# Performance work log

Hardware: AMD Instinct MI355X
Metric: run time of the kernel (lower is better)

The kernel has to match this reference:

```python
import jax, jax.numpy as jnp
import numpy as np

TWO_PI = 2.0 * np.pi
EPS = 1e-12  # torch F.normalize eps


def setup_inputs() -> dict:
    key = jax.random.key(0)
    ks = jax.random.split(key, 12)
    B, NS, G = 16, 128, 20000
    P, S, E, T = 200, 128, 128, 50
    return {
        "x_genes": jax.random.normal(ks[0], (B, NS, G), jnp.float32),
        "tissue_idx": jax.random.randint(ks[1], (B, NS), 0, T, jnp.int32),
        "pathway_idx": jax.random.randint(ks[2], (P, S), 0, G, jnp.int32),
        "W_proj": jax.random.normal(ks[3], (P, E, S), jnp.float32) * (1.0 / np.sqrt(S)),
        "b_proj": jax.random.normal(ks[4], (P, E), jnp.float32) * 0.02,
        "tissue_table": jax.random.normal(ks[5], (T, E), jnp.float32),
        "W1": jax.random.normal(ks[6], (E, 32), jnp.float32) * (1.0 / np.sqrt(E)),
        "b1": jax.random.normal(ks[7], (32,), jnp.float32) * 0.02,
        "W2": jax.random.normal(ks[8], (32, 2), jnp.float32) * (1.0 / np.sqrt(32)),
        "b2": jax.random.normal(ks[9], (2,), jnp.float32) * 0.02,
        "Wdec": jax.random.normal(ks[10], (2, G), jnp.float32) * (1.0 / np.sqrt(2.0)),
        "bdec": jax.random.normal(ks[11], (G,), jnp.float32) * 0.02,
    }


def _l2norm(v):
    n = jnp.sqrt(jnp.sum(v * v, axis=-1, keepdims=True))
    return v / jnp.maximum(n, EPS)


def reference(x_genes, tissue_idx, pathway_idx, W_proj, b_proj, tissue_table,
              W1, b1, W2, b2, Wdec, bdec):
    B, NS, G = x_genes.shape
    x = x_genes.reshape(-1, G)            # [N, G], N = B*NS
    t = tissue_idx.reshape(-1)            # [N]

    # Pathway tokenizer: gather gene subsets + per-pathway linear (grouped GEMM)
    xg = x[:, pathway_idx]                # [N, P, S]
    H = jax.nn.relu(jnp.einsum('nps,pes->npe', xg, W_proj) + b_proj)  # [N, P, E]

    # Single-query attention with tissue embedding as query
    Q = tissue_table[t]                   # [N, E]
    scale = 1.0 / np.sqrt(H.shape[-1])
    scores = jnp.einsum('ne,npe->np', Q, H) * scale   # [N, P]
    attn = jax.nn.softmax(scores, axis=-1)
    context = jnp.einsum('np,npe->ne', attn, H)       # [N, E]

    # to_latent MLP (dropout=0 / eval)
    h = jax.nn.relu(context @ W1 + b1)
    pc = h @ W2 + b2                      # [N, 2]
    pcn = _l2norm(pc)
    ang = jnp.remainder(jnp.arctan2(pcn[:, 1], pcn[:, 0]) + TWO_PI, TWO_PI)

    # decode + normalize
    rec = _l2norm(pcn @ Wdec + bdec)      # [N, G]

    return (pcn.reshape(B, NS, 2), ang.reshape(B, NS), rec.reshape(B, NS, G))
```

## Files before the change

kernel.cpp:

```cpp
#include <hip/hip_runtime.h>
#include <cmath>

#define GG 20000
#define NN 2048
#define PP 200
#define SS 128
#define EE 128
#define TN 128
#define NPAIR 100

typedef __bf16 bf16x8 __attribute__((ext_vector_type(8)));
typedef float f32x16 __attribute__((ext_vector_type(16)));
typedef unsigned short u16x8 __attribute__((ext_vector_type(8)));

__device__ __align__(16) unsigned g_xTi[(size_t)GG * NN];
__device__ __align__(16) unsigned short g_Wsw[(size_t)PP * 32768];
__device__ float g_ctxp[(size_t)NN * NPAIR * EE];
__device__ float g_mT[NPAIR * NN];
__device__ float g_lT[NPAIR * NN];

__device__ __forceinline__ unsigned short f2bf(float f) {
  unsigned u = __builtin_bit_cast(unsigned, f);
  return (unsigned short)((u + 0x7FFFu + ((u >> 16) & 1u)) >> 16);
}
__device__ __forceinline__ float bf2f(unsigned short h) {
  return __builtin_bit_cast(float, (unsigned)h << 16);
}
__device__ __forceinline__ unsigned packhl(float f) {
  unsigned short h = f2bf(f);
  unsigned short l = f2bf(f - bf2f(h));
  return (unsigned)h | ((unsigned)l << 16);
}

__global__ __launch_bounds__(256) void transpose_convert_kernel(
    const float* __restrict__ x)
{
  __shared__ float tile[64][65];
  const int g0 = blockIdx.x * 64;
  const int n0 = blockIdx.y * 64;
  const int t = threadIdx.x;
  {
    const int gq = t & 15, nl4 = t >> 4;
    #pragma unroll
    for (int k = 0; k < 4; ++k) {
      int nl = nl4 + 16 * k;
      int g = g0 + gq * 4;
      if (g + 3 < GG) {
        float4 v = *(const float4*)&x[(size_t)(n0 + nl) * GG + g];
        tile[gq * 4 + 0][nl] = v.x;
        tile[gq * 4 + 1][nl] = v.y;
        tile[gq * 4 + 2][nl] = v.z;
        tile[gq * 4 + 3][nl] = v.w;
      }
    }
  }
  __syncthreads();
  {
    const int nq = t & 15, gl4 = t >> 4;
    #pragma unroll
    for (int k = 0; k < 4; ++k) {
      int gl = gl4 + 16 * k;
      int g = g0 + gl;
      if (g < GG) {
        uint4 v;
        v.x = packhl(tile[gl][nq * 4 + 0]);
        v.y = packhl(tile[gl][nq * 4 + 1]);
        v.z = packhl(tile[gl][nq * 4 + 2]);
        v.w = packhl(tile[gl][nq * 4 + 3]);
        *(uint4*)&g_xTi[(size_t)g * NN + n0 + nq * 4] = v;
      }
    }
  }
}

__global__ __launch_bounds__(256) void wconvert_kernel(const float* __restrict__ Wp)
{
  unsigned v = blockIdx.x * 256 + threadIdx.x;
  const int si = v & 7;
  const int slp = (v >> 3) & 7;
  const int e = (v >> 6) & 127;
  const int ch = (v >> 13) & 1;
  const int p = v >> 14;
  const int slot = slp ^ (e & 7);
  const int s = ch * 64 + slot * 8 + si;
  float f = Wp[((size_t)p * EE + e) * SS + s];
  unsigned short h = f2bf(f);
  unsigned short l = f2bf(f - bf2f(h));
  size_t base = (size_t)(p * 2 + ch) * 16384 + e * 64 + slp * 8 + si;
  g_Wsw[base] = h;
  g_Wsw[base + 8192] = l;
}

__device__ __forceinline__ void load16(unsigned* xr, const int* sidx_lds,
                                       int sbase, int kh, int ncol) {
  #pragma unroll
  for (int ks2 = 0; ks2 < 2; ++ks2)
    #pragma unroll
    for (int j = 0; j < 8; ++j) {
      int s = (sbase + ks2) * 16 + kh * 8 + j;
      xr[ks2 * 8 + j] = g_xTi[(size_t)sidx_lds[s] * NN + ncol];
    }
}

__device__ __forceinline__ void compute2ks(const unsigned short* wb,
                                           const unsigned* xr, f32x16 (&acc)[4],
                                           int ksbase, int nl, int kh) {
  #pragma unroll
  for (int ks2 = 0; ks2 < 2; ++ks2) {
    const int ks = ksbase + ks2;
    const unsigned short* wAh = wb + (ks >> 2) * 16384;
    const unsigned short* wAl = wAh + 8192;
    u16x8 bhu, blu;
    #pragma unroll
    for (int j = 0; j < 8; ++j) {
      unsigned v = xr[ks2 * 8 + j];
      bhu[j] = (unsigned short)(v & 0xffffu);
      blu[j] = (unsigned short)(v >> 16);
    }
    bf16x8 bh = __builtin_bit_cast(bf16x8, bhu);
    bf16x8 bl = __builtin_bit_cast(bf16x8, blu);
    #pragma unroll
    for (int et = 0; et < 4; ++et) {
      const int e = et * 32 + nl;
      const int slp = ((ks & 3) * 2 + kh) ^ (e & 7);
      bf16x8 ah = __builtin_bit_cast(bf16x8, *(const uint4*)(wAh + e * 64 + slp * 8));
      bf16x8 al = __builtin_bit_cast(bf16x8, *(const uint4*)(wAl + e * 64 + slp * 8));
      acc[et] = __builtin_amdgcn_mfma_f32_32x32x16_bf16(ah, bh, acc[et], 0, 0, 0);
      acc[et] = __builtin_amdgcn_mfma_f32_32x32x16_bf16(ah, bl, acc[et], 0, 0, 0);
      acc[et] = __builtin_amdgcn_mfma_f32_32x32x16_bf16(al, bh, acc[et], 0, 0, 0);
    }
  }
}

__device__ __forceinline__ void pathway_body(
    int p, unsigned short* wbuf, int* sidx, float* sbp,
    const int* __restrict__ pidx, const float* __restrict__ bp,
    const float* __restrict__ tt, int tid_n,
    int t, int w, int ln, int nl, int kh, int ncol,
    f32x16 (&h)[4], float& s_out)
{
  __syncthreads();
  if (t < 128) sidx[t] = pidx[p * SS + t];
  else         sbp[t - 128] = bp[p * EE + (t - 128)];
  {
    const unsigned short* src = g_Wsw + (size_t)p * 32768 + w * 8192 + ln * 8;
    unsigned short* dst = wbuf + w * 8192;
    #pragma unroll
    for (int j = 0; j < 16; ++j) {
      __builtin_amdgcn_global_load_lds(
          (const __attribute__((address_space(1))) unsigned int*)(src + j * 512),
          (__attribute__((address_space(3))) unsigned int*)(dst + j * 512), 16, 0, 0);
    }
  }
  __syncthreads();

  #pragma unroll
  for (int et = 0; et < 4; ++et)
    #pragma unroll
    for (int r = 0; r < 16; ++r) h[et][r] = 0.f;

  unsigned xa[16], xb[16];
  load16(xa, sidx, 0, kh, ncol);
  load16(xb, sidx, 2, kh, ncol);
  compute2ks(wbuf, xa, h, 0, nl, kh);
  load16(xa, sidx, 4, kh, ncol);
  compute2ks(wbuf, xb, h, 2, nl, kh);
  load16(xb, sidx, 6, kh, ncol);
  compute2ks(wbuf, xa, h, 4, nl, kh);
  compute2ks(wbuf, xb, h, 6, nl, kh);

  const float4* qp = (const float4*)(tt + (size_t)tid_n * EE);
  float scr = 0.f;
  #pragma unroll
  for (int et = 0; et < 4; ++et)
    #pragma unroll
    for (int rq = 0; rq < 4; ++rq) {
      int e0 = et * 32 + rq * 8 + kh * 4;
      float4 q4 = qp[e0 >> 2];
      float4 b4 = *(const float4*)&sbp[e0];
      float h0 = fmaxf(h[et][rq * 4 + 0] + b4.x, 0.f);
      float h1 = fmaxf(h[et][rq * 4 + 1] + b4.y, 0.f);
      float h2 = fmaxf(h[et][rq * 4 + 2] + b4.z, 0.f);
      float h3 = fmaxf(h[et][rq * 4 + 3] + b4.w, 0.f);
      h[et][rq * 4 + 0] = h0; h[et][rq * 4 + 1] = h1;
      h[et][rq * 4 + 2] = h2; h[et][rq * 4 + 3] = h3;
      scr += h0 * q4.x + h1 * q4.y + h2 * q4.z + h3 * q4.w;
    }
  scr += __shfl_xor(scr, 32);
  s_out = scr * 0.08838834764831845f;
}

__global__ __launch_bounds__(256, 2) void proj_mfma_kernel(
    const int* __restrict__ tidx, const int* __restrict__ pidx,
    const float* __restrict__ bp, const float* __restrict__ tt)
{
  __shared__ __align__(16) unsigned short wbuf[32768];
  __shared__ int sidx[SS];
  __shared__ float sbp[EE];

  const int t = threadIdx.x;
  const int w = t >> 6;
  const int ln = t & 63;
  const int nl = ln & 31;
  const int kh = ln >> 5;
  const int n0 = blockIdx.x * TN;
  const int pair = blockIdx.y;
  const int ncol = n0 + w * 32 + nl;
  const int tid_n = tidx[ncol];

  f32x16 h0[4], h1[4];
  float s0, s1;
  pathway_body(pair * 2 + 0, wbuf, sidx, sbp, pidx, bp, tt, tid_n,
               t, w, ln, nl, kh, ncol, h0, s0);
  pathway_body(pair * 2 + 1, wbuf, sidx, sbp, pidx, bp, tt, tid_n,
               t, w, ln, nl, kh, ncol, h1, s1);

  const float m = fmaxf(s0, s1);
  const float w0 = expf(s0 - m);
  const float w1 = expf(s1 - m);
  const float lsum = w0 + w1;
  #pragma unroll
  for (int et = 0; et < 4; ++et)
    #pragma unroll
    for (int r = 0; r < 16; ++r)
      h0[et][r] = w0 * h0[et][r] + w1 * h1[et][r];

  __syncthreads();
  float* tb = ((float*)wbuf) + w * (32 * 128);
  #pragma unroll
  for (int et = 0; et < 4; ++et)
    #pragma unroll
    for (int rq = 0; rq < 4; ++rq) {
      int slot = et * 8 + rq * 2 + kh;
      float4 v = make_float4(h0[et][rq * 4 + 0], h0[et][rq * 4 + 1],
                             h0[et][rq * 4 + 2], h0[et][rq * 4 + 3]);
      *(float4*)&tb[nl * 128 + ((slot ^ nl) << 2)] = v;
    }
  __syncthreads();
  {
    const int rrow = ln >> 1, eh = (ln & 1) * 16;
    const int nn = n0 + w * 32 + rrow;
    float* dst = g_ctxp + ((size_t)nn * NPAIR + pair) * EE + eh * 4;
    const float* srcrow = tb + rrow * 128;
    #pragma unroll
    for (int k = 0; k < 16; ++k) {
      int slot = eh + k;
      *(float4*)&dst[k * 4] = *(const float4*)&srcrow[(slot ^ rrow) << 2];
    }
  }
  if (ln < 32) {
    g_mT[pair * NN + ncol] = m;
    g_lT[pair * NN + ncol] = lsum;
  }
}

__global__ __launch_bounds__(256) void combine_rec_kernel(
    const float* __restrict__ W1, const float* __restrict__ b1,
    const float* __restrict__ W2, const float* __restrict__ b2,
    const float* __restrict__ Wdec, const float* __restrict__ bdec,
    float* __restrict__ out)
{
  const int n = blockIdx.x;
  const int t = threadIdx.x;
  __shared__ float ws[NPAIR];
  __shared__ float ctx2[2][EE];
  __shared__ float r1[4], r2[4];
  __shared__ float hsh[32];
  __shared__ float qsh[2];
  __shared__ float red[4];

  float mv = (t < NPAIR) ? g_mT[t * NN + n] : -1e30f;
  float lv = (t < NPAIR) ? g_lT[t * NN + n] : 0.f;
  float M = mv;
  #pragma unroll
  for (int off = 32; off >= 1; off >>= 1) M = fmaxf(M, __shfl_xor(M, off));
  if ((t & 63) == 0) r1[t >> 6] = M;
  __syncthreads();
  M = fmaxf(fmaxf(r1[0], r1[1]), fmaxf(r1[2], r1[3]));
  float wv = (t < NPAIR) ? expf(mv - M) : 0.f;
  if (t < NPAIR) ws[t] = wv;
  float Lp = wv * lv;
  #pragma unroll
  for (int off = 32; off >= 1; off >>= 1) Lp += __shfl_xor(Lp, off);
  if ((t & 63) == 0) r2[t >> 6] = Lp;
  __syncthreads();
  const float L = r2[0] + r2[1] + r2[2] + r2[3];

  {
    const int e = t & 127, hf = t >> 7;
    const float* base = g_ctxp + ((size_t)n * NPAIR + hf * 50) * EE + e;
    float c = 0.f;
    #pragma unroll 5
    for (int s = 0; s < 50; ++s) c += ws[hf * 50 + s] * base[(size_t)s * EE];
    ctx2[hf][e] = c;
  }
  __syncthreads();
  const float invL = 1.f / L;
  if (t < 32) {
    float h = 0.f;
    for (int e = 0; e < EE; ++e) h += (ctx2[0][e] + ctx2[1][e]) * W1[e * 32 + t];
    hsh[t] = fmaxf(h * invL + b1[t], 0.f);
  }
  __syncthreads();
  if (t == 0) {
    float p0 = b2[0], p1 = b2[1];
    #pragma unroll
    for (int k = 0; k < 32; ++k) { p0 += hsh[k] * W2[k * 2]; p1 += hsh[k] * W2[k * 2 + 1]; }
    float inv = 1.f / fmaxf(sqrtf(p0 * p0 + p1 * p1), 1e-12f);
    float q0 = p0 * inv, q1 = p1 * inv;
    const float PI2 = 6.2831853071795864769f;
    float ang = atan2f(q1, q0) + PI2;
    if (ang >= PI2) ang -= PI2;
    out[n * 2 + 0] = q0;
    out[n * 2 + 1] = q1;
    out[2 * NN + n] = ang;
    qsh[0] = q0; qsh[1] = q1;
  }
  __syncthreads();
  const float q0 = qsh[0], q1 = qsh[1];

  float ss = 0.f;
  for (int i = t; i < GG / 4; i += 256) {
    float4 w0 = *(const float4*)&Wdec[i * 4];
    float4 w1 = *(const float4*)&Wdec[GG + i * 4];
    float4 bd = *(const float4*)&bdec[i * 4];
    float v0 = q0 * w0.x + q1 * w1.x + bd.x;
    float v1 = q0 * w0.y + q1 * w1.y + bd.y;
    float v2 = q0 * w0.z + q1 * w1.z + bd.z;
    float v3 = q0 * w0.w + q1 * w1.w + bd.w;
    ss += v0 * v0 + v1 * v1 + v2 * v2 + v3 * v3;
  }
  #pragma unroll
  for (int off = 32; off >= 1; off >>= 1) ss += __shfl_xor(ss, off);
  if ((t & 63) == 0) red[t >> 6] = ss;
  __syncthreads();
  const float inv = 1.f / fmaxf(sqrtf(red[0] + red[1] + red[2] + red[3]), 1e-12f);

  float* orec = out + 3 * NN + (size_t)n * GG;
  for (int i = t; i < GG / 4; i += 256) {
    float4 w0 = *(const float4*)&Wdec[i * 4];
    float4 w1 = *(const float4*)&Wdec[GG + i * 4];
    float4 bd = *(const float4*)&bdec[i * 4];
    float4 o;
    o.x = (q0 * w0.x + q1 * w1.x + bd.x) * inv;
    o.y = (q0 * w0.y + q1 * w1.y + bd.y) * inv;
    o.z = (q0 * w0.z + q1 * w1.z + bd.z) * inv;
    o.w = (q0 * w0.w + q1 * w1.w + bd.w) * inv;
    *(float4*)&orec[i * 4] = o;
  }
}

extern "C" void kernel_launch(void* const* d_in, const int* in_sizes, int n_in,
                              void* d_out, int out_size, void* d_ws, size_t ws_size,
                              hipStream_t stream) {
  (void)in_sizes; (void)n_in; (void)out_size; (void)d_ws; (void)ws_size;
  const float* x    = (const float*)d_in[0];
  const int*   tidx = (const int*)  d_in[1];
  const int*   pidx = (const int*)  d_in[2];
  const float* Wp   = (const float*)d_in[3];
  const float* bp   = (const float*)d_in[4];
  const float* tt   = (const float*)d_in[5];
  const float* W1   = (const float*)d_in[6];
  const float* b1   = (const float*)d_in[7];
  const float* W2   = (const float*)d_in[8];
  const float* b2   = (const float*)d_in[9];
  const float* Wdec = (const float*)d_in[10];
  const float* bdec = (const float*)d_in[11];
  float* out = (float*)d_out;

  dim3 gridT((GG + 63) / 64, NN / 64, 1);
  transpose_convert_kernel<<<gridT, 256, 0, stream>>>(x);
  wconvert_kernel<<<(PP * 16384) / 256, 256, 0, stream>>>(Wp);

  dim3 gridA(NN / TN, NPAIR, 1);
  proj_mfma_kernel<<<gridA, 256, 0, stream>>>(tidx, pidx, bp, tt);

  combine_rec_kernel<<<NN, 256, 0, stream>>>(W1, b1, W2, b2, Wdec, bdec, out);
}
```

Baseline: 320.6 us.

## Process eight pathways per block with online softmax to shrink partial context buffer

Each projection block now loops over eight pathways instead of two, keeping a running max, sum and weighted context in registers (online softmax). The partial-context buffer and max/sum arrays drop from 100 to 25 slices per sample, which cuts global write traffic in the projection kernel and read traffic in the combine kernel. The cost is a grid with a quarter as many blocks (16x25 = 400), so there is less parallelism for the MI355X's CUs and each block runs longer and more serially.

```diff
diff --git a/kernel.cpp b/kernel.cpp
--- a/kernel.cpp
+++ b/kernel.cpp
@@ -7,7 +7,8 @@
 #define SS 128
 #define EE 128
 #define TN 128
-#define NPAIR 100
+#define TPP 8
+#define NOCT 25
 
 typedef __bf16 bf16x8 __attribute__((ext_vector_type(8)));
 typedef float f32x16 __attribute__((ext_vector_type(16)));
@@ -15,9 +16,9 @@
 
 __device__ __align__(16) unsigned g_xTi[(size_t)GG * NN];
 __device__ __align__(16) unsigned short g_Wsw[(size_t)PP * 32768];
-__device__ float g_ctxp[(size_t)NN * NPAIR * EE];
-__device__ float g_mT[NPAIR * NN];
-__device__ float g_lT[NPAIR * NN];
+__device__ float g_ctxp[(size_t)NN * NOCT * EE];
+__device__ float g_mT[NOCT * NN];
+__device__ float g_lT[NOCT * NN];
 
 __device__ __forceinline__ unsigned short f2bf(float f) {
   unsigned u = __builtin_bit_cast(unsigned, f);
@@ -204,26 +205,33 @@
   const int nl = ln & 31;
   const int kh = ln >> 5;
   const int n0 = blockIdx.x * TN;
-  const int pair = blockIdx.y;
+  const int oct = blockIdx.y;
   const int ncol = n0 + w * 32 + nl;
   const int tid_n = tidx[ncol];
 
-  f32x16 h0[4], h1[4];
-  float s0, s1;
-  pathway_body(pair * 2 + 0, wbuf, sidx, sbp, pidx, bp, tt, tid_n,
-               t, w, ln, nl, kh, ncol, h0, s0);
-  pathway_body(pair * 2 + 1, wbuf, sidx, sbp, pidx, bp, tt, tid_n,
-               t, w, ln, nl, kh, ncol, h1, s1);
-
-  const float m = fmaxf(s0, s1);
-  const float w0 = expf(s0 - m);
-  const float w1 = expf(s1 - m);
-  const float lsum = w0 + w1;
+  f32x16 ctx[4];
   #pragma unroll
   for (int et = 0; et < 4; ++et)
     #pragma unroll
-    for (int r = 0; r < 16; ++r)
-      h0[et][r] = w0 * h0[et][r] + w1 * h1[et][r];
+    for (int r = 0; r < 16; ++r) ctx[et][r] = 0.f;
+  float m_r = -1e30f, l_r = 0.f;
+
+  f32x16 h[4];
+  float s;
+  for (int pp = 0; pp < TPP; ++pp) {
+    pathway_body(oct * TPP + pp, wbuf, sidx, sbp, pidx, bp, tt, tid_n,
+                 t, w, ln, nl, kh, ncol, h, s);
+    const float mn = fmaxf(m_r, s);
+    const float f = expf(m_r - mn);
+    const float wg = expf(s - mn);
+    l_r = l_r * f + wg;
+    m_r = mn;
+    #pragma unroll
+    for (int et = 0; et < 4; ++et)
+      #pragma unroll
+      for (int r = 0; r < 16; ++r)
+        ctx[et][r] = ctx[et][r] * f + wg * h[et][r];
+  }
 
   __syncthreads();
   float* tb = ((float*)wbuf) + w * (32 * 128);
@@ -232,15 +240,15 @@
     #pragma unroll
     for (int rq = 0; rq < 4; ++rq) {
       int slot = et * 8 + rq * 2 + kh;
-      float4 v = make_float4(h0[et][rq * 4 + 0], h0[et][rq * 4 + 1],
-                             h0[et][rq * 4 + 2], h0[et][rq * 4 + 3]);
+      float4 v = make_float4(ctx[et][rq * 4 + 0], ctx[et][rq * 4 + 1],
+                             ctx[et][rq * 4 + 2], ctx[et][rq * 4 + 3]);
       *(float4*)&tb[nl * 128 + ((slot ^ nl) << 2)] = v;
     }
   __syncthreads();
   {
     const int rrow = ln >> 1, eh = (ln & 1) * 16;
     const int nn = n0 + w * 32 + rrow;
-    float* dst = g_ctxp + ((size_t)nn * NPAIR + pair) * EE + eh * 4;
+    float* dst = g_ctxp + ((size_t)nn * NOCT + oct) * EE + eh * 4;
     const float* srcrow = tb + rrow * 128;
     #pragma unroll
     for (int k = 0; k < 16; ++k) {
@@ -249,8 +257,8 @@
     }
   }
   if (ln < 32) {
-    g_mT[pair * NN + ncol] = m;
-    g_lT[pair * NN + ncol] = lsum;
+    g_mT[oct * NN + ncol] = m_r;
+    g_lT[oct * NN + ncol] = l_r;
   }
 }
 
@@ -262,23 +270,23 @@
 {
   const int n = blockIdx.x;
   const int t = threadIdx.x;
-  __shared__ float ws[NPAIR];
+  __shared__ float ws[NOCT];
   __shared__ float ctx2[2][EE];
   __shared__ float r1[4], r2[4];
   __shared__ float hsh[32];
   __shared__ float qsh[2];
   __shared__ float red[4];
 
-  float mv = (t < NPAIR) ? g_mT[t * NN + n] : -1e30f;
-  float lv = (t < NPAIR) ? g_lT[t * NN + n] : 0.f;
+  float mv = (t < NOCT) ? g_mT[t * NN + n] : -1e30f;
+  float lv = (t < NOCT) ? g_lT[t * NN + n] : 0.f;
   float M = mv;
   #pragma unroll
   for (int off = 32; off >= 1; off >>= 1) M = fmaxf(M, __shfl_xor(M, off));
   if ((t & 63) == 0) r1[t >> 6] = M;
   __syncthreads();
   M = fmaxf(fmaxf(r1[0], r1[1]), fmaxf(r1[2], r1[3]));
-  float wv = (t < NPAIR) ? expf(mv - M) : 0.f;
-  if (t < NPAIR) ws[t] = wv;
+  float wv = (t < NOCT) ? expf(mv - M) : 0.f;
+  if (t < NOCT) ws[t] = wv;
   float Lp = wv * lv;
   #pragma unroll
   for (int off = 32; off >= 1; off >>= 1) Lp += __shfl_xor(Lp, off);
@@ -288,10 +296,10 @@
 
   {
     const int e = t & 127, hf = t >> 7;
-    const float* base = g_ctxp + ((size_t)n * NPAIR + hf * 50) * EE + e;
+    const int sA = hf ? 13 : 0, sB = hf ? NOCT : 13;
+    const float* base = g_ctxp + ((size_t)n * NOCT + sA) * EE + e;
     float c = 0.f;
-    #pragma unroll 5
-    for (int s = 0; s < 50; ++s) c += ws[hf * 50 + s] * base[(size_t)s * EE];
+    for (int s = sA; s < sB; ++s) c += ws[s] * base[(size_t)(s - sA) * EE];
     ctx2[hf][e] = c;
   }
   __syncthreads();
@@ -372,7 +380,7 @@
   transpose_convert_kernel<<<gridT, 256, 0, stream>>>(x);
   wconvert_kernel<<<(PP * 16384) / 256, 256, 0, stream>>>(Wp);
 
-  dim3 gridA(NN / TN, NPAIR, 1);
+  dim3 gridA(NN / TN, NOCT, 1);
   proj_mfma_kernel<<<gridA, 256, 0, stream>>>(tidx, pidx, bp, tt);
 
   combine_rec_kernel<<<NN, 256, 0, stream>>>(W1, b1, W2, b2, Wdec, bdec, out);
```

Result: faster. 286.2 us (-10.7%).
